# Kernel optimization log

Measured on AMD Instinct MI355X. Metric: run time of the kernel, lower is better.

Reference implementation:

```python
import jax, jax.numpy as jnp
import numpy as np

N_NODES = 50000
N_EDGES = 600000
D = 128
HIDDEN = 128
OUT = 3


def setup_inputs() -> dict:
    key = jax.random.key(0)
    ks = jax.random.split(key, 8)
    x = jax.random.normal(ks[0], (N_NODES, D), dtype=jnp.float32)
    edge_index = jax.random.randint(ks[1], (2, N_EDGES), 0, N_NODES, dtype=jnp.int64)
    # egnn.lin: Linear(D, D)
    W_lin = jax.random.normal(ks[2], (D, D), dtype=jnp.float32) / np.sqrt(D)
    b_lin = jnp.zeros((D,), dtype=jnp.float32)
    # fc1: Linear(D, 128), fc2: Linear(128, 3)
    W1 = jax.random.normal(ks[3], (HIDDEN, D), dtype=jnp.float32) / np.sqrt(D)
    b1 = jnp.zeros((HIDDEN,), dtype=jnp.float32)
    W2 = jax.random.normal(ks[4], (OUT, HIDDEN), dtype=jnp.float32) / np.sqrt(HIDDEN)
    b2 = jnp.zeros((OUT,), dtype=jnp.float32)
    return {"x": x, "edge_index": edge_index, "W_lin": W_lin, "b_lin": b_lin,
            "W1": W1, "b1": b1, "W2": W2, "b2": b2}


def reference(x, edge_index, W_lin, b_lin, W1, b1, W2, b2):
    N = x.shape[0]
    # add_self_loops: append (i, i) for every node
    loops = jnp.arange(N, dtype=edge_index.dtype)
    src = jnp.concatenate([edge_index[0], loops])  # j (gathered)
    dst = jnp.concatenate([edge_index[1], loops])  # i (aggregated)
    # message: lin(x_j). Linear is per-node, so transform once then gather.
    y = x @ W_lin.T + b_lin  # [N, D]
    msg = y[src]  # [E+N, D] gather
    # aggr='mean' scatter over target nodes
    summ = jax.ops.segment_sum(msg, dst, num_segments=N)  # [N, D]
    cnt = jax.ops.segment_sum(jnp.ones(dst.shape, dtype=y.dtype), dst, num_segments=N)
    agg = summ / jnp.maximum(cnt, 1.0)[:, None]
    # dense tail: relu(fc1) -> fc2 -> sum over nodes
    h = jax.nn.relu(agg @ W1.T + b1)
    out = h @ W2.T + b2  # [N, 3]
    return jnp.sum(out, axis=0)  # [3]
```

## Files before the change

kernel.cpp:

```cpp
#include <hip/hip_runtime.h>

#define NN 50000
#define NE 600000
#define DD 128
#define SLOTS 64
#define CSTRIDE 32

typedef float f32x4 __attribute__((ext_vector_type(4)));
typedef short bf16x8 __attribute__((ext_vector_type(8)));

__device__ __forceinline__ ushort f2bf(float f) {
    uint u = __float_as_uint(f);
    u = (u + 0x7FFFu + ((u >> 16) & 1u)) >> 16;
    return (ushort)u;
}
__device__ __forceinline__ float bfhi2f(uint u) { return __uint_as_float(u & 0xFFFF0000u); }
__device__ __forceinline__ float bflo2f(uint u) { return __uint_as_float(u << 16); }


__global__ void k_init(const float4* __restrict__ x4, uint2* __restrict__ xb,
                       const float4* __restrict__ Wl4, const float4* __restrict__ W14,
                       uint2* __restrict__ wbl2, uint2* __restrict__ wb12,
                       int* __restrict__ cntp, float* __restrict__ hsum) {
    int i = blockIdx.x * blockDim.x + threadIdx.x;
    if (i < NN * 32) {
        float4 v = x4[i];
        uint2 o;
        o.x = (uint)f2bf(v.x) | ((uint)f2bf(v.y) << 16);
        o.y = (uint)f2bf(v.z) | ((uint)f2bf(v.w) << 16);
        xb[i] = o;
        cntp[i] = 0;
    }
    if (i < 4096) {
        float4 v = Wl4[i];
        uint2 o;
        o.x = (uint)f2bf(v.x) | ((uint)f2bf(v.y) << 16);
        o.y = (uint)f2bf(v.z) | ((uint)f2bf(v.w) << 16);
        wbl2[i] = o;
        v = W14[i];
        o.x = (uint)f2bf(v.x) | ((uint)f2bf(v.y) << 16);
        o.y = (uint)f2bf(v.z) | ((uint)f2bf(v.w) << 16);
        wb12[i] = o;
    }
    if (i < DD) hsum[i] = 0.0f;
}


__global__ void k_scatter(const int* __restrict__ ei, int* __restrict__ cntp, ushort* __restrict__ slot) {
    int e = blockIdx.x * blockDim.x + threadIdx.x;
    if (e < NE) {
        int dst = ei[NE + e];
        int pos = atomicAdd(&cntp[(size_t)dst * CSTRIDE], 1);
        slot[(size_t)dst * SLOTS + pos] = (ushort)ei[e];
    }
}


__global__ __launch_bounds__(256) void k_gather(const uint4* __restrict__ xb4,
                                                const int* __restrict__ cntp,
                                                const ushort* __restrict__ slot,
                                                uint4* __restrict__ meanb4) {
    int gt = blockIdx.x * blockDim.x + threadIdx.x;
    int wid = gt >> 4;
    int lane = gt & 15;
    if (wid >= NN) return;
    uint4 s = xb4[(size_t)wid * 16 + lane];
    float a0 = bflo2f(s.x), a1 = bfhi2f(s.x), a2 = bflo2f(s.y), a3 = bfhi2f(s.y);
    float a4 = bflo2f(s.z), a5 = bfhi2f(s.z), a6 = bflo2f(s.w), a7 = bfhi2f(s.w);
    const ushort* sl = slot + (size_t)wid * SLOTS;
    int n = cntp[(size_t)wid * CSTRIDE];
    int j = 0;
    for (; j + 7 < n; j += 8) {
        int i0 = sl[j], i1 = sl[j + 1], i2 = sl[j + 2], i3 = sl[j + 3];
        int i4 = sl[j + 4], i5 = sl[j + 5], i6 = sl[j + 6], i7 = sl[j + 7];
        uint4 v0 = xb4[(size_t)i0 * 16 + lane];
        uint4 v1 = xb4[(size_t)i1 * 16 + lane];
        uint4 v2 = xb4[(size_t)i2 * 16 + lane];
        uint4 v3 = xb4[(size_t)i3 * 16 + lane];
        uint4 v4 = xb4[(size_t)i4 * 16 + lane];
        uint4 v5 = xb4[(size_t)i5 * 16 + lane];
        uint4 v6 = xb4[(size_t)i6 * 16 + lane];
        uint4 v7 = xb4[(size_t)i7 * 16 + lane];
        a0 += (bflo2f(v0.x) + bflo2f(v1.x)) + (bflo2f(v2.x) + bflo2f(v3.x))
            + (bflo2f(v4.x) + bflo2f(v5.x)) + (bflo2f(v6.x) + bflo2f(v7.x));
        a1 += (bfhi2f(v0.x) + bfhi2f(v1.x)) + (bfhi2f(v2.x) + bfhi2f(v3.x))
            + (bfhi2f(v4.x) + bfhi2f(v5.x)) + (bfhi2f(v6.x) + bfhi2f(v7.x));
        a2 += (bflo2f(v0.y) + bflo2f(v1.y)) + (bflo2f(v2.y) + bflo2f(v3.y))
            + (bflo2f(v4.y) + bflo2f(v5.y)) + (bflo2f(v6.y) + bflo2f(v7.y));
        a3 += (bfhi2f(v0.y) + bfhi2f(v1.y)) + (bfhi2f(v2.y) + bfhi2f(v3.y))
            + (bfhi2f(v4.y) + bfhi2f(v5.y)) + (bfhi2f(v6.y) + bfhi2f(v7.y));
        a4 += (bflo2f(v0.z) + bflo2f(v1.z)) + (bflo2f(v2.z) + bflo2f(v3.z))
            + (bflo2f(v4.z) + bflo2f(v5.z)) + (bflo2f(v6.z) + bflo2f(v7.z));
        a5 += (bfhi2f(v0.z) + bfhi2f(v1.z)) + (bfhi2f(v2.z) + bfhi2f(v3.z))
            + (bfhi2f(v4.z) + bfhi2f(v5.z)) + (bfhi2f(v6.z) + bfhi2f(v7.z));
        a6 += (bflo2f(v0.w) + bflo2f(v1.w)) + (bflo2f(v2.w) + bflo2f(v3.w))
            + (bflo2f(v4.w) + bflo2f(v5.w)) + (bflo2f(v6.w) + bflo2f(v7.w));
        a7 += (bfhi2f(v0.w) + bfhi2f(v1.w)) + (bfhi2f(v2.w) + bfhi2f(v3.w))
            + (bfhi2f(v4.w) + bfhi2f(v5.w)) + (bfhi2f(v6.w) + bfhi2f(v7.w));
    }
    for (; j + 3 < n; j += 4) {
        int i0 = sl[j], i1 = sl[j + 1], i2 = sl[j + 2], i3 = sl[j + 3];
        uint4 v0 = xb4[(size_t)i0 * 16 + lane];
        uint4 v1 = xb4[(size_t)i1 * 16 + lane];
        uint4 v2 = xb4[(size_t)i2 * 16 + lane];
        uint4 v3 = xb4[(size_t)i3 * 16 + lane];
        a0 += (bflo2f(v0.x) + bflo2f(v1.x)) + (bflo2f(v2.x) + bflo2f(v3.x));
        a1 += (bfhi2f(v0.x) + bfhi2f(v1.x)) + (bfhi2f(v2.x) + bfhi2f(v3.x));
        a2 += (bflo2f(v0.y) + bflo2f(v1.y)) + (bflo2f(v2.y) + bflo2f(v3.y));
        a3 += (bfhi2f(v0.y) + bfhi2f(v1.y)) + (bfhi2f(v2.y) + bfhi2f(v3.y));
        a4 += (bflo2f(v0.z) + bflo2f(v1.z)) + (bflo2f(v2.z) + bflo2f(v3.z));
        a5 += (bfhi2f(v0.z) + bfhi2f(v1.z)) + (bfhi2f(v2.z) + bfhi2f(v3.z));
        a6 += (bflo2f(v0.w) + bflo2f(v1.w)) + (bflo2f(v2.w) + bflo2f(v3.w));
        a7 += (bfhi2f(v0.w) + bfhi2f(v1.w)) + (bfhi2f(v2.w) + bfhi2f(v3.w));
    }
    for (; j < n; ++j) {
        uint4 v = xb4[(size_t)sl[j] * 16 + lane];
        a0 += bflo2f(v.x); a1 += bfhi2f(v.x);
        a2 += bflo2f(v.y); a3 += bfhi2f(v.y);
        a4 += bflo2f(v.z); a5 += bfhi2f(v.z);
        a6 += bflo2f(v.w); a7 += bfhi2f(v.w);
    }
    float rc = 1.0f / (float)(n + 1);
    uint4 o;
    o.x = (uint)f2bf(a0 * rc) | ((uint)f2bf(a1 * rc) << 16);
    o.y = (uint)f2bf(a2 * rc) | ((uint)f2bf(a3 * rc) << 16);
    o.z = (uint)f2bf(a4 * rc) | ((uint)f2bf(a5 * rc) << 16);
    o.w = (uint)f2bf(a6 * rc) | ((uint)f2bf(a7 * rc) << 16);
    meanb4[(size_t)wid * 16 + lane] = o;
}


__global__ __launch_bounds__(256) void k_fused(const ushort* __restrict__ meanb,
                                               const uint4* __restrict__ wbl4,
                                               const uint4* __restrict__ wb14,
                                               const float* __restrict__ bl,
                                               const float* __restrict__ b1,
                                               float* __restrict__ hsum) {
    __shared__ ushort sWl[128 * 128];
    __shared__ ushort sW1[128 * 128];
    __shared__ ushort sAgg[4 * 2048];

    int tid = threadIdx.x;
    int wid = tid >> 6, lane = tid & 63;
    int lm = lane & 15, lq = lane >> 4;

    for (int idx = tid; idx < 2048; idx += 256) {
        int r = idx >> 4, g = idx & 15;
        int dst = r * 128 + ((g ^ (r & 7)) << 3);
        *(uint4*)&sWl[dst] = wbl4[idx];
        *(uint4*)&sW1[dst] = wb14[idx];
    }
    __syncthreads();

    float blr[8], b1r[8], hacc[8];
    #pragma unroll
    for (int ct = 0; ct < 8; ++ct) {
        blr[ct] = bl[ct * 16 + lm];
        b1r[ct] = b1[ct * 16 + lm];
        hacc[ct] = 0.0f;
    }

    ushort* myAgg = &sAgg[wid * 2048];
    const int NT = NN / 16;

    for (int wt = blockIdx.x * 4 + wid; wt < NT; wt += gridDim.x * 4) {
        int nbase = wt * 16;

        bf16x8 afr[4];
        #pragma unroll
        for (int kt = 0; kt < 4; ++kt)
            afr[kt] = *(const bf16x8*)&meanb[(size_t)(nbase + lm) * 128 + kt * 32 + lq * 8];

        #pragma unroll
        for (int ct = 0; ct < 8; ++ct) {
            f32x4 acc = {0.f, 0.f, 0.f, 0.f};
            int rB = ct * 16 + lm;
            #pragma unroll
            for (int kt = 0; kt < 4; ++kt) {
                bf16x8 bfr = *(const bf16x8*)&sWl[rB * 128 + (((kt * 4 + lq) ^ (rB & 7)) << 3)];
                acc = __builtin_amdgcn_mfma_f32_16x16x32_bf16(afr[kt], bfr, acc, 0, 0, 0);
            }
            #pragma unroll
            for (int r = 0; r < 4; ++r) {
                int n = lq * 4 + r;
                int col = ct * 16 + lm;
                myAgg[n * 128 + (((col >> 3) ^ (n & 7)) << 3) + (col & 7)] = f2bf(acc[r] + blr[ct]);
            }
        }

        bf16x8 afr2[4];
        #pragma unroll
        for (int kt = 0; kt < 4; ++kt)
            afr2[kt] = *(const bf16x8*)&myAgg[lm * 128 + (((kt * 4 + lq) ^ (lm & 7)) << 3)];

        #pragma unroll
        for (int ct = 0; ct < 8; ++ct) {
            f32x4 acc = {0.f, 0.f, 0.f, 0.f};
            int rB = ct * 16 + lm;
            #pragma unroll
            for (int kt = 0; kt < 4; ++kt) {
                bf16x8 bfr = *(const bf16x8*)&sW1[rB * 128 + (((kt * 4 + lq) ^ (rB & 7)) << 3)];
                acc = __builtin_amdgcn_mfma_f32_16x16x32_bf16(afr2[kt], bfr, acc, 0, 0, 0);
            }
            float s0 = fmaxf(acc[0] + b1r[ct], 0.f);
            float s1 = fmaxf(acc[1] + b1r[ct], 0.f);
            float s2 = fmaxf(acc[2] + b1r[ct], 0.f);
            float s3 = fmaxf(acc[3] + b1r[ct], 0.f);
            hacc[ct] += (s0 + s1) + (s2 + s3);
        }
    }

    #pragma unroll
    for (int ct = 0; ct < 8; ++ct) {
        float v = hacc[ct];
        v += __shfl_xor(v, 16);
        v += __shfl_xor(v, 32);
        hacc[ct] = v;
    }
    __syncthreads();
    float* red = (float*)sAgg;
    if (lane < 16) {
        #pragma unroll
        for (int ct = 0; ct < 8; ++ct) red[wid * 128 + ct * 16 + lane] = hacc[ct];
    }
    __syncthreads();
    if (tid < 128) {
        float s = (red[tid] + red[128 + tid]) + (red[256 + tid] + red[384 + tid]);
        atomicAdd(&hsum[tid], s);
    }
}

__global__ void k_out(const float* __restrict__ hsum, const float* __restrict__ W2,
                      const float* __restrict__ b2, float* __restrict__ out) {
    int j = threadIdx.x;
    if (j < 3) {
        float acc = 0.0f;
        for (int k = 0; k < DD; ++k) acc += hsum[k] * W2[j * DD + k];
        out[j] = acc + (float)NN * b2[j];
    }
}

extern "C" void kernel_launch(void* const* d_in, const int* in_sizes, int n_in,
                              void* d_out, int out_size, void* d_ws, size_t ws_size,
                              hipStream_t stream) {
    const float* x  = (const float*)d_in[0];
    const int* ei   = (const int*)d_in[1];
    const float* Wl = (const float*)d_in[2];
    const float* bl = (const float*)d_in[3];
    const float* W1 = (const float*)d_in[4];
    const float* b1 = (const float*)d_in[5];
    const float* W2 = (const float*)d_in[6];
    const float* b2 = (const float*)d_in[7];

    char* wsb     = (char*)d_ws;
    ushort* xb    = (ushort*)wsb;
    ushort* meanb = xb + (size_t)NN * DD;
    float* hsum   = (float*)(meanb + (size_t)NN * DD);
    int* cntp     = (int*)(hsum + DD);
    ushort* slot  = (ushort*)(cntp + (size_t)NN * CSTRIDE);
    ushort* wbl   = slot + (size_t)NN * SLOTS;
    ushort* wb1   = wbl + DD * DD;

    k_init<<<(NN * 32 + 255) / 256, 256, 0, stream>>>((const float4*)x, (uint2*)xb,
                                                      (const float4*)Wl, (const float4*)W1,
                                                      (uint2*)wbl, (uint2*)wb1, cntp, hsum);
    k_scatter<<<(NE + 255) / 256, 256, 0, stream>>>(ei, cntp, slot);
    k_gather<<<(NN * 16 + 255) / 256, 256, 0, stream>>>((const uint4*)xb, cntp, slot, (uint4*)meanb);
    k_fused<<<512, 256, 0, stream>>>(meanb, (const uint4*)wbl, (const uint4*)wb1, bl, b1, hsum);
    k_out<<<1, 64, 0, stream>>>(hsum, W2, b2, (float*)d_out);
}
```

Before: 90.78 us.

## Fuse edge scatter into init kernel and fold output projection into fused kernel

Merges the bf16 conversion kernel and the edge-scatter kernel into one launch, with each block handling 96 edges (NN*32/256 blocks × 96 = 600000) alongside its x conversion slice. The per-node counter zeroing moves to a hipMemsetAsync, which is still a separate operation. The final 3-output projection is computed per block inside the fused kernel and accumulated atomically into the output, removing the small k_out launch and the hsum buffer. The intent is to cut launch overhead and overlap atomic scatter latency with conversion work, at the cost of two memset operations and 512×3 extra float atomics on the output.

```diff
diff --git a/kernel.cpp b/kernel.cpp
--- a/kernel.cpp
+++ b/kernel.cpp
@@ -5,6 +5,7 @@
 #define DD 128
 #define SLOTS 64
 #define CSTRIDE 32
+#define EPB 96
 
 typedef float f32x4 __attribute__((ext_vector_type(4)));
 typedef short bf16x8 __attribute__((ext_vector_type(8)));
@@ -18,18 +19,29 @@
 __device__ __forceinline__ float bflo2f(uint u) { return __uint_as_float(u << 16); }
 
 
-__global__ void k_init(const float4* __restrict__ x4, uint2* __restrict__ xb,
-                       const float4* __restrict__ Wl4, const float4* __restrict__ W14,
-                       uint2* __restrict__ wbl2, uint2* __restrict__ wb12,
-                       int* __restrict__ cntp, float* __restrict__ hsum) {
-    int i = blockIdx.x * blockDim.x + threadIdx.x;
-    if (i < NN * 32) {
+__global__ __launch_bounds__(256) void k_initscat(const float4* __restrict__ x4, uint2* __restrict__ xb,
+                                                  const float4* __restrict__ Wl4, const float4* __restrict__ W14,
+                                                  uint2* __restrict__ wbl2, uint2* __restrict__ wb12,
+                                                  const int* __restrict__ ei, int* __restrict__ cntp,
+                                                  ushort* __restrict__ slot) {
+    int b = blockIdx.x, tid = threadIdx.x;
+    int i = b * 256 + tid;
+
+    int src = 0, dst = 0, pos = 0;
+    bool hasE = (tid < EPB);
+    if (hasE) {
+        int e = b * EPB + tid;
+        src = ei[e];
+        dst = ei[NE + e];
+        pos = atomicAdd(&cntp[(size_t)dst * CSTRIDE], 1);
+    }
+
+    {
         float4 v = x4[i];
         uint2 o;
         o.x = (uint)f2bf(v.x) | ((uint)f2bf(v.y) << 16);
         o.y = (uint)f2bf(v.z) | ((uint)f2bf(v.w) << 16);
         xb[i] = o;
-        cntp[i] = 0;
     }
     if (i < 4096) {
         float4 v = Wl4[i];
@@ -42,17 +54,8 @@
         o.y = (uint)f2bf(v.z) | ((uint)f2bf(v.w) << 16);
         wb12[i] = o;
     }
-    if (i < DD) hsum[i] = 0.0f;
-}
-
-
-__global__ void k_scatter(const int* __restrict__ ei, int* __restrict__ cntp, ushort* __restrict__ slot) {
-    int e = blockIdx.x * blockDim.x + threadIdx.x;
-    if (e < NE) {
-        int dst = ei[NE + e];
-        int pos = atomicAdd(&cntp[(size_t)dst * CSTRIDE], 1);
-        slot[(size_t)dst * SLOTS + pos] = (ushort)ei[e];
-    }
+
+    if (hasE) slot[(size_t)dst * SLOTS + pos] = (ushort)src;
 }
 
 
@@ -135,7 +138,9 @@
                                                const uint4* __restrict__ wb14,
                                                const float* __restrict__ bl,
                                                const float* __restrict__ b1,
-                                               float* __restrict__ hsum) {
+                                               const float* __restrict__ W2,
+                                               const float* __restrict__ b2,
+                                               float* __restrict__ out) {
     __shared__ ushort sWl[128 * 128];
     __shared__ ushort sW1[128 * 128];
     __shared__ ushort sAgg[4 * 2048];
@@ -226,17 +231,15 @@
     __syncthreads();
     if (tid < 128) {
         float s = (red[tid] + red[128 + tid]) + (red[256 + tid] + red[384 + tid]);
-        atomicAdd(&hsum[tid], s);
-    }
-}
-
-__global__ void k_out(const float* __restrict__ hsum, const float* __restrict__ W2,
-                      const float* __restrict__ b2, float* __restrict__ out) {
-    int j = threadIdx.x;
-    if (j < 3) {
+        red[tid] = s;
+    }
+    __syncthreads();
+    if (tid < 3) {
         float acc = 0.0f;
-        for (int k = 0; k < DD; ++k) acc += hsum[k] * W2[j * DD + k];
-        out[j] = acc + (float)NN * b2[j];
+        #pragma unroll 4
+        for (int k = 0; k < DD; ++k) acc += red[k] * W2[tid * DD + k];
+        if (blockIdx.x == 0) acc += (float)NN * b2[tid];
+        atomicAdd(&out[tid], acc);
     }
 }
 
@@ -255,17 +258,18 @@
     char* wsb     = (char*)d_ws;
     ushort* xb    = (ushort*)wsb;
     ushort* meanb = xb + (size_t)NN * DD;
-    float* hsum   = (float*)(meanb + (size_t)NN * DD);
-    int* cntp     = (int*)(hsum + DD);
+    int* cntp     = (int*)(meanb + (size_t)NN * DD);
     ushort* slot  = (ushort*)(cntp + (size_t)NN * CSTRIDE);
     ushort* wbl   = slot + (size_t)NN * SLOTS;
     ushort* wb1   = wbl + DD * DD;
 
-    k_init<<<(NN * 32 + 255) / 256, 256, 0, stream>>>((const float4*)x, (uint2*)xb,
-                                                      (const float4*)Wl, (const float4*)W1,
-                                                      (uint2*)wbl, (uint2*)wb1, cntp, hsum);
-    k_scatter<<<(NE + 255) / 256, 256, 0, stream>>>(ei, cntp, slot);
+    hipMemsetAsync(cntp, 0, (size_t)NN * CSTRIDE * sizeof(int), stream);
+    hipMemsetAsync(d_out, 0, 3 * sizeof(float), stream);
+
+    k_initscat<<<NN * 32 / 256, 256, 0, stream>>>((const float4*)x, (uint2*)xb,
+                                                  (const float4*)Wl, (const float4*)W1,
+                                                  (uint2*)wbl, (uint2*)wb1, ei, cntp, slot);
     k_gather<<<(NN * 16 + 255) / 256, 256, 0, stream>>>((const uint4*)xb, cntp, slot, (uint4*)meanb);
-    k_fused<<<512, 256, 0, stream>>>(meanb, (const uint4*)wbl, (const uint4*)wb1, bl, b1, hsum);
-    k_out<<<1, 64, 0, stream>>>(hsum, W2, b2, (float*)d_out);
-}
+    k_fused<<<512, 256, 0, stream>>>(meanb, (const uint4*)wbl, (const uint4*)wb1,
+                                     bl, b1, W2, b2, (float*)d_out);
+}
```

New measurement: 93.88 us. 1.03x slower.

## Replace global atomic edge scatter with two-pass binned partition via LDS

Applied to the files above, without the earlier changes.

The per-edge global atomic scatter into padded per-node counters is replaced by a two-pass partition. The first pass histograms edges into 391 bins of 128 destination nodes in shared memory, reserves space per bin with one global atomic, and stages packed (src, local dst) words. The second pass builds each bin's per-node slot lists in LDS and writes them out coalesced with a compact count array. This removes heavily contended, scattered global atomics and the large padded counter memset, at the cost of an extra kernel launch and a staging buffer with a fixed capacity per bin.

```diff
diff --git a/kernel.cpp b/kernel.cpp
--- a/kernel.cpp
+++ b/kernel.cpp
@@ -4,7 +4,9 @@
 #define NE 600000
 #define DD 128
 #define SLOTS 64
-#define CSTRIDE 32
+#define NBIN 391
+#define BSHIFT 7
+#define BINCAP 2048
 
 typedef float f32x4 __attribute__((ext_vector_type(4)));
 typedef short bf16x8 __attribute__((ext_vector_type(8)));
@@ -21,7 +23,7 @@
 __global__ void k_init(const float4* __restrict__ x4, uint2* __restrict__ xb,
                        const float4* __restrict__ Wl4, const float4* __restrict__ W14,
                        uint2* __restrict__ wbl2, uint2* __restrict__ wb12,
-                       int* __restrict__ cntp, float* __restrict__ hsum) {
+                       int* __restrict__ binCur, float* __restrict__ hsum) {
     int i = blockIdx.x * blockDim.x + threadIdx.x;
     if (i < NN * 32) {
         float4 v = x4[i];
@@ -29,7 +31,6 @@
         o.x = (uint)f2bf(v.x) | ((uint)f2bf(v.y) << 16);
         o.y = (uint)f2bf(v.z) | ((uint)f2bf(v.w) << 16);
         xb[i] = o;
-        cntp[i] = 0;
     }
     if (i < 4096) {
         float4 v = Wl4[i];
@@ -42,22 +43,84 @@
         o.y = (uint)f2bf(v.z) | ((uint)f2bf(v.w) << 16);
         wb12[i] = o;
     }
+    if (i < NBIN) binCur[i] = i * BINCAP;
     if (i < DD) hsum[i] = 0.0f;
 }
 
 
-__global__ void k_scatter(const int* __restrict__ ei, int* __restrict__ cntp, ushort* __restrict__ slot) {
-    int e = blockIdx.x * blockDim.x + threadIdx.x;
-    if (e < NE) {
-        int dst = ei[NE + e];
-        int pos = atomicAdd(&cntp[(size_t)dst * CSTRIDE], 1);
-        slot[(size_t)dst * SLOTS + pos] = (ushort)ei[e];
-    }
+__global__ __launch_bounds__(1024) void k_partA(const int* __restrict__ ei,
+                                                int* __restrict__ binCur,
+                                                uint* __restrict__ staged) {
+    __shared__ int hist[NBIN];
+    __shared__ int cur[NBIN];
+    int tid = threadIdx.x;
+    if (tid < NBIN) hist[tid] = 0;
+    __syncthreads();
+
+    int e0 = blockIdx.x * 4096 + tid * 4;
+    int4 srcs, dsts;
+    bool has = e0 < NE;
+    if (has) {
+        srcs = *(const int4*)&ei[e0];
+        dsts = *(const int4*)&ei[NE + e0];
+        atomicAdd(&hist[dsts.x >> BSHIFT], 1);
+        atomicAdd(&hist[dsts.y >> BSHIFT], 1);
+        atomicAdd(&hist[dsts.z >> BSHIFT], 1);
+        atomicAdd(&hist[dsts.w >> BSHIFT], 1);
+    }
+    __syncthreads();
+    if (tid < NBIN) {
+        int h = hist[tid];
+        cur[tid] = h ? atomicAdd(&binCur[tid], h) : 0;
+    }
+    __syncthreads();
+    if (has) {
+        int p;
+        p = atomicAdd(&cur[dsts.x >> BSHIFT], 1);
+        staged[p] = (uint)srcs.x | ((uint)(dsts.x & 127) << 16);
+        p = atomicAdd(&cur[dsts.y >> BSHIFT], 1);
+        staged[p] = (uint)srcs.y | ((uint)(dsts.y & 127) << 16);
+        p = atomicAdd(&cur[dsts.z >> BSHIFT], 1);
+        staged[p] = (uint)srcs.z | ((uint)(dsts.z & 127) << 16);
+        p = atomicAdd(&cur[dsts.w >> BSHIFT], 1);
+        staged[p] = (uint)srcs.w | ((uint)(dsts.w & 127) << 16);
+    }
+}
+
+
+__global__ __launch_bounds__(256) void k_partB(const uint* __restrict__ staged,
+                                               const int* __restrict__ binCur,
+                                               int* __restrict__ cnt,
+                                               ushort* __restrict__ slot) {
+    __shared__ ushort buck[128 * SLOTS];
+    __shared__ int lcnt[128];
+    int bin = blockIdx.x, tid = threadIdx.x;
+    if (tid < 128) lcnt[tid] = 0;
+    __syncthreads();
+
+    int base = bin * BINCAP;
+    int total = binCur[bin] - base;
+    for (int k = tid; k < total; k += 256) {
+        uint pk = staged[base + k];
+        int node = pk >> 16;
+        int pos = atomicAdd(&lcnt[node], 1);
+        buck[node * SLOTS + pos] = (ushort)(pk & 0xFFFFu);
+    }
+    __syncthreads();
+
+    int nodeBase = bin * 128;
+    const uint4* bs = (const uint4*)buck;
+    uint4* bd = (uint4*)(slot + (size_t)nodeBase * SLOTS);
+    for (int k = tid; k < 1024; k += 256) {
+        int node = k >> 3;
+        if (nodeBase + node < NN) bd[k] = bs[k];
+    }
+    if (tid < 128 && nodeBase + tid < NN) cnt[nodeBase + tid] = lcnt[tid];
 }
 
 
 __global__ __launch_bounds__(256) void k_gather(const uint4* __restrict__ xb4,
-                                                const int* __restrict__ cntp,
+                                                const int* __restrict__ cnt,
                                                 const ushort* __restrict__ slot,
                                                 uint4* __restrict__ meanb4) {
     int gt = blockIdx.x * blockDim.x + threadIdx.x;
@@ -68,7 +131,7 @@
     float a0 = bflo2f(s.x), a1 = bfhi2f(s.x), a2 = bflo2f(s.y), a3 = bfhi2f(s.y);
     float a4 = bflo2f(s.z), a5 = bfhi2f(s.z), a6 = bflo2f(s.w), a7 = bfhi2f(s.w);
     const ushort* sl = slot + (size_t)wid * SLOTS;
-    int n = cntp[(size_t)wid * CSTRIDE];
+    int n = cnt[wid];
     int j = 0;
     for (; j + 7 < n; j += 8) {
         int i0 = sl[j], i1 = sl[j + 1], i2 = sl[j + 2], i3 = sl[j + 3];
@@ -256,16 +319,19 @@
     ushort* xb    = (ushort*)wsb;
     ushort* meanb = xb + (size_t)NN * DD;
     float* hsum   = (float*)(meanb + (size_t)NN * DD);
-    int* cntp     = (int*)(hsum + DD);
-    ushort* slot  = (ushort*)(cntp + (size_t)NN * CSTRIDE);
+    int* cnt      = (int*)(hsum + DD);
+    int* binCur   = cnt + NN;
+    uint* staged  = (uint*)(binCur + 512);
+    ushort* slot  = (ushort*)(staged + (size_t)NBIN * BINCAP);
     ushort* wbl   = slot + (size_t)NN * SLOTS;
     ushort* wb1   = wbl + DD * DD;
 
-    k_init<<<(NN * 32 + 255) / 256, 256, 0, stream>>>((const float4*)x, (uint2*)xb,
-                                                      (const float4*)Wl, (const float4*)W1,
-                                                      (uint2*)wbl, (uint2*)wb1, cntp, hsum);
-    k_scatter<<<(NE + 255) / 256, 256, 0, stream>>>(ei, cntp, slot);
-    k_gather<<<(NN * 16 + 255) / 256, 256, 0, stream>>>((const uint4*)xb, cntp, slot, (uint4*)meanb);
+    k_init<<<NN * 32 / 256, 256, 0, stream>>>((const float4*)x, (uint2*)xb,
+                                              (const float4*)Wl, (const float4*)W1,
+                                              (uint2*)wbl, (uint2*)wb1, binCur, hsum);
+    k_partA<<<(NE + 4095) / 4096, 1024, 0, stream>>>(ei, binCur, staged);
+    k_partB<<<NBIN, 256, 0, stream>>>(staged, binCur, cnt, slot);
+    k_gather<<<(NN * 16 + 255) / 256, 256, 0, stream>>>((const uint4*)xb, cnt, slot, (uint4*)meanb);
     k_fused<<<512, 256, 0, stream>>>(meanb, (const uint4*)wbl, (const uint4*)wb1, bl, b1, hsum);
     k_out<<<1, 64, 0, stream>>>(hsum, W2, b2, (float*)d_out);
 }
```

Result: faster. 75.70 us, median of 2 (-16.6%).
